# Optimization experiments

Hardware: AMD Instinct MI355X
Metric: run time of the kernel (lower is better)

The kernel has to match this reference:

```python
import jax, jax.numpy as jnp
import numpy as np

EPS = 1e-9


def _pairwise_sqdist(x1, x2):
    # x1: (B,n,3), x2: (B,m,3) -> (B,n,m) squared euclidean distances
    s1 = jnp.sum(x1 * x1, axis=-1)
    s2 = jnp.sum(x2 * x2, axis=-1)
    cross = jnp.einsum('bnd,bmd->bnm', x1, x2)
    return jnp.maximum(s1[:, :, None] + s2[:, None, :] - 2.0 * cross, 0.0)


def _approxmatch(x1, x2):
    # Faithful port of the approxmatch CUDA kernel (Fan et al. EMD approx).
    B, n, _ = x1.shape
    m = x2.shape[1]
    if n >= m:
        multiL, multiR = 1.0, float(n // m)   # integer division as in CUDA
    else:
        multiL, multiR = float(m // n), 1.0
    dist = _pairwise_sqdist(x1, x2)  # (B,n,m)
    # j = 7 .. -1 -> level = -4^j ; j = -2 -> level = 0  (10 sweeps total)
    levels = jnp.concatenate([
        -(4.0 ** jnp.arange(7, -2, -1, dtype=jnp.float32)),
        jnp.zeros((1,), jnp.float32)])
    match0 = jnp.zeros((B, n, m), jnp.float32)
    remainL0 = jnp.full((B, n), multiL, jnp.float32)
    remainR0 = jnp.full((B, m), multiR, jnp.float32)

    def body(carry, level):
        match, remainL, remainR = carry
        e = jnp.exp(level * dist)                              # (B,n,m)
        suml = EPS + jnp.einsum('bnm,bm->bn', e, remainR)
        ratioL = remainL / suml                                # (B,n)
        sumr = remainR * jnp.einsum('bnm,bn->bm', e, ratioL)   # (B,m)
        consumption = jnp.minimum(remainR / (sumr + EPS), 1.0)
        ratioR = consumption * remainR                         # (B,m)
        remainR = jnp.maximum(0.0, remainR - sumr)
        w = e * ratioL[:, :, None] * ratioR[:, None, :]        # flow k->l
        match = match + w
        remainL = jnp.maximum(0.0, remainL - jnp.sum(w, axis=-1))
        return (match, remainL, remainR), None

    (match, _, _), _ = jax.lax.scan(body, (match0, remainL0, remainR0), levels)
    return match, dist


def setup_inputs() -> dict:
    key = jax.random.key(0)
    k1, k2 = jax.random.split(key)
    B, N = 4, 4096
    xyz1 = jax.random.normal(k1, (B, 3, N), dtype=jnp.float32)
    xyz2 = jax.random.normal(k2, (B, 3, N), dtype=jnp.float32)
    return {"xyz1": xyz1, "xyz2": xyz2}


def reference(xyz1, xyz2):
    # transpose=True: BCN -> BNC
    x1 = jnp.transpose(xyz1, (0, 2, 1))
    x2 = jnp.transpose(xyz2, (0, 2, 1))
    match, dist = _approxmatch(x1, x2)
    d = jnp.sqrt(jnp.maximum(dist, 1e-20))
    cost = jnp.sum(match * d, axis=(1, 2))            # (B,)
    emd = cost / min(x1.shape[1], x2.shape[1])
    return jnp.mean(emd)                               # reduce_mean=True
```

## Files before the change

kernel.cpp:

```cpp
#include <hip/hip_runtime.h>


#define NPTS 4096
#define BATCH 4
#define EMD_EPS 1e-9f
#define TILE 1024
#define RPW 2
#define THREADS 256
#define RPB 8
#define NBLK (NPTS / RPB)

typedef float v2f __attribute__((ext_vector_type(2)));

__device__ __forceinline__ float fexp2(float x) {
#if __has_builtin(__builtin_amdgcn_exp2f)
    return __builtin_amdgcn_exp2f(x);
#else
    return exp2f(x);
#endif
}
__device__ __forceinline__ float fsqrt(float x) {
#if __has_builtin(__builtin_amdgcn_sqrtf)
    return __builtin_amdgcn_sqrtf(x);
#else
    return __sqrtf(x);
#endif
}

__device__ __forceinline__ float wave_reduce(float v) {
    v += __shfl_xor(v, 32);
    v += __shfl_xor(v, 16);
    v += __shfl_xor(v, 8);
    v += __shfl_xor(v, 4);
    v += __shfl_xor(v, 2);
    v += __shfl_xor(v, 1);
    return v;
}

__global__ __launch_bounds__(THREADS, 6) void k_ratioL0(
        const float* __restrict__ xyz1, const float* __restrict__ xyz2,
        float* __restrict__ ratioL, float* __restrict__ remainL,
        float* __restrict__ remainR, float ls2) {
    const int b = blockIdx.y;
    const int tid = threadIdx.x;
    const int wave = tid >> 6;
    const int lane = tid & 63;
    const int row0 = blockIdx.x * RPB + wave * RPW;

    const float* x1 = xyz1 + b * 3 * NPTS;
    const float* x2 = xyz2 + b * 3 * NPTS;
    const float2* x2x = (const float2*)(x2);
    const float2* x2y = (const float2*)(x2 + NPTS);
    const float2* x2z = (const float2*)(x2 + 2 * NPTS);

    float px[RPW], py[RPW], pz[RPW];
    v2f acc[RPW];
#pragma unroll
    for (int r = 0; r < RPW; ++r) {
        px[r] = x1[row0 + r];
        py[r] = x1[NPTS + row0 + r];
        pz[r] = x1[2 * NPTS + row0 + r];
        acc[r] = (v2f)(0.0f);
    }
    __shared__ float4 sA[TILE / 2];
    __shared__ float2 sZ[TILE / 2];

    for (int c0 = 0; c0 < NPTS; c0 += TILE) {
        __syncthreads();
        for (int i = tid; i < TILE / 2; i += THREADS) {
            int e = c0 / 2 + i;
            float2 xx = x2x[e], yy = x2y[e];
            sA[i] = make_float4(xx.x, xx.y, yy.x, yy.y);
            sZ[i] = x2z[e];
        }
        __syncthreads();
#pragma unroll 2
        for (int j = 0; j < TILE / 128; ++j) {
            float4 a = sA[lane + 64 * j];
            float2 z = sZ[lane + 64 * j];
            v2f ax = {a.x, a.y}, ay = {a.z, a.w}, az = {z.x, z.y};
#pragma unroll
            for (int r = 0; r < RPW; ++r) {
                v2f dx = px[r] - ax, dy = py[r] - ay, dz = pz[r] - az;
                v2f d = dx * dx + dy * dy + dz * dz;
                v2f sd = ls2 * d;
                v2f e2 = {fexp2(sd.x), fexp2(sd.y)};
                acc[r] += e2;
            }
        }
    }
#pragma unroll
    for (int r = 0; r < RPW; ++r) {
        float s = wave_reduce(acc[r].x + acc[r].y);
        if (lane == 0) {
            int idx = b * NPTS + row0 + r;
            ratioL[idx] = 1.0f / (EMD_EPS + s);
            remainL[idx] = 1.0f;
            remainR[idx] = 1.0f;
        }
    }
}

__global__ __launch_bounds__(THREADS, 6) void k_ratioR(
        const float* __restrict__ xyz1, const float* __restrict__ xyz2,
        const float* __restrict__ ratioL, float* __restrict__ ratioR,
        float* __restrict__ remainR, float ls2) {
    const int b = blockIdx.y;
    const int tid = threadIdx.x;
    const int wave = tid >> 6;
    const int lane = tid & 63;
    const int col0 = blockIdx.x * RPB + wave * RPW;

    const float* x1 = xyz1 + b * 3 * NPTS;
    const float* x2 = xyz2 + b * 3 * NPTS;
    const float2* x1x = (const float2*)(x1);
    const float2* x1y = (const float2*)(x1 + NPTS);
    const float2* x1z = (const float2*)(x1 + 2 * NPTS);
    const float2* wLv = (const float2*)(ratioL + b * NPTS);

    float px[RPW], py[RPW], pz[RPW];
    v2f acc[RPW];
#pragma unroll
    for (int r = 0; r < RPW; ++r) {
        px[r] = x2[col0 + r];
        py[r] = x2[NPTS + col0 + r];
        pz[r] = x2[2 * NPTS + col0 + r];
        acc[r] = (v2f)(0.0f);
    }
    __shared__ float4 sA[TILE / 2];
    __shared__ float4 sB[TILE / 2];

    for (int c0 = 0; c0 < NPTS; c0 += TILE) {
        __syncthreads();
        for (int i = tid; i < TILE / 2; i += THREADS) {
            int e = c0 / 2 + i;
            float2 xx = x1x[e], yy = x1y[e], zz = x1z[e], ww = wLv[e];
            sA[i] = make_float4(xx.x, xx.y, yy.x, yy.y);
            sB[i] = make_float4(zz.x, zz.y, ww.x, ww.y);
        }
        __syncthreads();
#pragma unroll 2
        for (int j = 0; j < TILE / 128; ++j) {
            float4 a = sA[lane + 64 * j];
            float4 bq = sB[lane + 64 * j];
            v2f ax = {a.x, a.y}, ay = {a.z, a.w};
            v2f az = {bq.x, bq.y}, aw = {bq.z, bq.w};
#pragma unroll
            for (int r = 0; r < RPW; ++r) {
                v2f dx = px[r] - ax, dy = py[r] - ay, dz = pz[r] - az;
                v2f d = dx * dx + dy * dy + dz * dz;
                v2f sd = ls2 * d;
                v2f e2 = {fexp2(sd.x), fexp2(sd.y)};
                acc[r] += e2 * aw;
            }
        }
    }
#pragma unroll
    for (int r = 0; r < RPW; ++r) {
        float s = wave_reduce(acc[r].x + acc[r].y);
        if (lane == 0) {
            int idx = b * NPTS + col0 + r;
            float rv = remainR[idx];
            float sumr = rv * s;
            float cons = fminf(rv / (sumr + EMD_EPS), 1.0f);
            ratioR[idx] = cons * rv;
            remainR[idx] = fmaxf(0.0f, rv - sumr);
        }
    }
}

template <bool SQ>
__global__ __launch_bounds__(THREADS, 6) void k_cost_fused(
        const float* __restrict__ xyz1, const float* __restrict__ xyz2,
        float* __restrict__ ratioL, const float* __restrict__ ratioR,
        float* __restrict__ remainL, const float* __restrict__ remainR,
        float* __restrict__ cost_part, float ls2, float ls2n, int initCost) {
    const int b = blockIdx.y;
    const int tid = threadIdx.x;
    const int wave = tid >> 6;
    const int lane = tid & 63;
    const int row0 = blockIdx.x * RPB + wave * RPW;

    const float* x1 = xyz1 + b * 3 * NPTS;
    const float* x2 = xyz2 + b * 3 * NPTS;
    const float2* x2x = (const float2*)(x2);
    const float2* x2y = (const float2*)(x2 + NPTS);
    const float2* x2z = (const float2*)(x2 + 2 * NPTS);
    const float2* wRv = (const float2*)(ratioR + b * NPTS);
    const float2* w2v = (const float2*)(remainR + b * NPTS);

    float px[RPW], py[RPW], pz[RPW];
    v2f acc_a[RPW], acc_c[RPW], acc_s[RPW];
#pragma unroll
    for (int r = 0; r < RPW; ++r) {
        px[r] = x1[row0 + r];
        py[r] = x1[NPTS + row0 + r];
        pz[r] = x1[2 * NPTS + row0 + r];
        acc_a[r] = (v2f)(0.0f);
        acc_c[r] = (v2f)(0.0f);
        acc_s[r] = (v2f)(0.0f);
    }
    __shared__ float4 sA[TILE / 2];
    __shared__ float4 sB[TILE / 2];
    __shared__ float2 sC[TILE / 2];
    __shared__ float s_cost[THREADS / 64];

    for (int c0 = 0; c0 < NPTS; c0 += TILE) {
        __syncthreads();
        for (int i = tid; i < TILE / 2; i += THREADS) {
            int e = c0 / 2 + i;
            float2 xx = x2x[e], yy = x2y[e], zz = x2z[e], wr = wRv[e];
            sA[i] = make_float4(xx.x, xx.y, yy.x, yy.y);
            sB[i] = make_float4(zz.x, zz.y, wr.x, wr.y);
            sC[i] = w2v[e];
        }
        __syncthreads();
#pragma unroll 2
        for (int j = 0; j < TILE / 128; ++j) {
            float4 a = sA[lane + 64 * j];
            float4 bq = sB[lane + 64 * j];
            float2 c = sC[lane + 64 * j];
            v2f ax = {a.x, a.y}, ay = {a.z, a.w};
            v2f az = {bq.x, bq.y}, wr = {bq.z, bq.w};
            v2f cw = {c.x, c.y};
#pragma unroll
            for (int r = 0; r < RPW; ++r) {
                v2f dx = px[r] - ax, dy = py[r] - ay, dz = pz[r] - az;
                v2f d = dx * dx + dy * dy + dz * dz;
                v2f er;
                if (SQ) {
                    v2f sd = ls2n * d;
                    v2f e2 = {fexp2(sd.x), fexp2(sd.y)};
                    acc_s[r] += e2 * cw;
                    v2f e4 = e2 * e2;
                    er = (e4 * e4) * wr;
                } else {
                    v2f sd = ls2 * d;
                    v2f e1 = {fexp2(sd.x), fexp2(sd.y)};
                    er = e1 * wr;
                    acc_s[r] += cw;
                }
                acc_a[r] += er;
                v2f sq = {fsqrt(d.x), fsqrt(d.y)};
                acc_c[r] += er * sq;
            }
        }
    }
    float wcost = 0.0f;
#pragma unroll
    for (int r = 0; r < RPW; ++r) {
        float sa = wave_reduce(acc_a[r].x + acc_a[r].y);
        float sc = wave_reduce(acc_c[r].x + acc_c[r].y);
        float ss = wave_reduce(acc_s[r].x + acc_s[r].y);
        if (lane == 0) {
            int idx = b * NPTS + row0 + r;
            float rl = ratioL[idx];
            float rem = fmaxf(0.0f, remainL[idx] - rl * sa);
            remainL[idx] = rem;
            ratioL[idx] = rem / (EMD_EPS + ss);
            wcost = fmaf(rl, sc, wcost);
        }
    }
    if (lane == 0) s_cost[wave] = wcost;
    __syncthreads();
    if (tid == 0) {
        float t = s_cost[0] + s_cost[1] + s_cost[2] + s_cost[3];
        int ci = b * NBLK + blockIdx.x;
        cost_part[ci] = (initCost ? t : cost_part[ci] + t);
    }
}

__global__ void k_sum_ratioL(const float* __restrict__ ratioL, float* __restrict__ S_L) {
    const int b = blockIdx.x;
    const int tid = threadIdx.x;
    float s = 0.0f;
    for (int i = tid; i < NPTS; i += 256) s += ratioL[b * NPTS + i];
    s = wave_reduce(s);
    __shared__ float sw[4];
    if ((tid & 63) == 0) sw[tid >> 6] = s;
    __syncthreads();
    if (tid == 0) S_L[b] = sw[0] + sw[1] + sw[2] + sw[3];
}

__global__ __launch_bounds__(THREADS, 6) void k_cost_l0(
        const float* __restrict__ xyz1, const float* __restrict__ xyz2,
        const float* __restrict__ ratioL, const float* __restrict__ remainR,
        const float* __restrict__ S_L, float* __restrict__ cost_part) {
    const int b = blockIdx.y;
    const int tid = threadIdx.x;
    const int wave = tid >> 6;
    const int lane = tid & 63;
    const int row0 = blockIdx.x * RPB + wave * RPW;
    const float sL = S_L[b];

    const float* x1 = xyz1 + b * 3 * NPTS;
    const float* x2 = xyz2 + b * 3 * NPTS;
    const float2* x2x = (const float2*)(x2);
    const float2* x2y = (const float2*)(x2 + NPTS);
    const float2* x2z = (const float2*)(x2 + 2 * NPTS);
    const float2* wRv = (const float2*)(remainR + b * NPTS);

    float px[RPW], py[RPW], pz[RPW];
    v2f acc_c[RPW];
#pragma unroll
    for (int r = 0; r < RPW; ++r) {
        px[r] = x1[row0 + r];
        py[r] = x1[NPTS + row0 + r];
        pz[r] = x1[2 * NPTS + row0 + r];
        acc_c[r] = (v2f)(0.0f);
    }
    __shared__ float4 sA[TILE / 2];
    __shared__ float4 sB[TILE / 2];
    __shared__ float s_cost[THREADS / 64];

    for (int c0 = 0; c0 < NPTS; c0 += TILE) {
        __syncthreads();
        for (int i = tid; i < TILE / 2; i += THREADS) {
            int e = c0 / 2 + i;
            float2 xx = x2x[e], yy = x2y[e], zz = x2z[e], rv = wRv[e];
            float wr0 = fminf(rv.x / (rv.x * sL + EMD_EPS), 1.0f) * rv.x;
            float wr1 = fminf(rv.y / (rv.y * sL + EMD_EPS), 1.0f) * rv.y;
            sA[i] = make_float4(xx.x, xx.y, yy.x, yy.y);
            sB[i] = make_float4(zz.x, zz.y, wr0, wr1);
        }
        __syncthreads();
#pragma unroll 2
        for (int j = 0; j < TILE / 128; ++j) {
            float4 a = sA[lane + 64 * j];
            float4 bq = sB[lane + 64 * j];
            v2f ax = {a.x, a.y}, ay = {a.z, a.w};
            v2f az = {bq.x, bq.y}, wr = {bq.z, bq.w};
#pragma unroll
            for (int r = 0; r < RPW; ++r) {
                v2f dx = px[r] - ax, dy = py[r] - ay, dz = pz[r] - az;
                v2f d = dx * dx + dy * dy + dz * dz;
                v2f sq = {fsqrt(d.x), fsqrt(d.y)};
                acc_c[r] += wr * sq;
            }
        }
    }
    float wcost = 0.0f;
#pragma unroll
    for (int r = 0; r < RPW; ++r) {
        float sc = wave_reduce(acc_c[r].x + acc_c[r].y);
        if (lane == 0)
            wcost = fmaf(ratioL[b * NPTS + row0 + r], sc, wcost);
    }
    if (lane == 0) s_cost[wave] = wcost;
    __syncthreads();
    if (tid == 0) {
        float t = s_cost[0] + s_cost[1] + s_cost[2] + s_cost[3];
        cost_part[b * NBLK + blockIdx.x] += t;
    }
}

__global__ void k_final(const float* __restrict__ cost_part, float* __restrict__ out) {
    const int tid = threadIdx.x;
    float s = 0.0f;
    for (int i = tid; i < BATCH * NBLK; i += 256) s += cost_part[i];
    s = wave_reduce(s);
    __shared__ float sw[4];
    if ((tid & 63) == 0) sw[tid >> 6] = s;
    __syncthreads();
    if (tid == 0) out[0] = (sw[0] + sw[1] + sw[2] + sw[3]) / ((float)NPTS * (float)BATCH);
}

extern "C" void kernel_launch(void* const* d_in, const int* in_sizes, int n_in,
                              void* d_out, int out_size, void* d_ws, size_t ws_size,
                              hipStream_t stream) {
    const float* xyz1 = (const float*)d_in[0];
    const float* xyz2 = (const float*)d_in[1];
    float* out = (float*)d_out;

    const int BN = BATCH * NPTS;
    float* ws = (float*)d_ws;
    float* remainL  = ws;
    float* remainR  = ws + 1 * BN;
    float* ratioL   = ws + 2 * BN;
    float* ratioR   = ws + 3 * BN;
    float* cost_part = ws + 4 * BN;
    float* S_L      = cost_part + BATCH * NBLK;

    static const float levels[10] = {
        -16384.0f, -4096.0f, -1024.0f, -256.0f, -64.0f,
        -16.0f, -4.0f, -1.0f, -0.25f, 0.0f};
    float ls2[10];
    for (int t = 0; t < 10; ++t)
        ls2[t] = (float)(levels[t] * 1.4426950408889634);

    dim3 grid(NBLK, BATCH);

    k_ratioL0<<<grid, THREADS, 0, stream>>>(xyz1, xyz2, ratioL, remainL, remainR, ls2[0]);
    for (int t = 0; t < 8; ++t) {
        k_ratioR<<<grid, THREADS, 0, stream>>>(xyz1, xyz2, ratioL, ratioR, remainR, ls2[t]);
        k_cost_fused<true><<<grid, THREADS, 0, stream>>>(xyz1, xyz2, ratioL, ratioR,
                                                         remainL, remainR, cost_part,
                                                         ls2[t], ls2[t + 1], t == 0 ? 1 : 0);
    }
    k_ratioR<<<grid, THREADS, 0, stream>>>(xyz1, xyz2, ratioL, ratioR, remainR, ls2[8]);
    k_cost_fused<false><<<grid, THREADS, 0, stream>>>(xyz1, xyz2, ratioL, ratioR,
                                                      remainL, remainR, cost_part,
                                                      ls2[8], 0.0f, 0);
    k_sum_ratioL<<<BATCH, 256, 0, stream>>>(ratioL, S_L);
    k_cost_l0<<<grid, THREADS, 0, stream>>>(xyz1, xyz2, ratioL, remainR, S_L, cost_part);
    k_final<<<1, 256, 0, stream>>>(cost_part, out);
}
```

Baseline: 565.4 us.

## Cull negligible exp terms wave-wide and double rows per wave

Adds wave-uniform culling of exp2 evaluations in the first few high-magnitude level sweeps: when every lane's scaled distance is below a threshold, the exp, and optionally the cost and sqrt terms, are skipped because they would underflow to zero or be negligible. Separately, rows per wave go from 2 to 4 (rows per block 8 to 16), which improves reuse of the shared-memory tiles, and launch bounds are relaxed to 4 blocks per CU. The partial cull threshold drops terms that are small but not exactly zero, which slightly changes numerics. The extra per-step wave votes add branch overhead when little can be culled.

After: 527.5 us. 1.07x faster.

```diff
diff --git a/kernel.cpp b/kernel.cpp
--- a/kernel.cpp
+++ b/kernel.cpp
@@ -5,10 +5,13 @@
 #define BATCH 4
 #define EMD_EPS 1e-9f
 #define TILE 1024
-#define RPW 2
+#define RPW 4
 #define THREADS 256
-#define RPB 8
+#define RPB 16
 #define NBLK (NPTS / RPB)
+
+#define CULL_FULL -160.0f
+#define CULL_PART -40.0f
 
 typedef float v2f __attribute__((ext_vector_type(2)));
 
@@ -37,7 +40,7 @@
     return v;
 }
 
-__global__ __launch_bounds__(THREADS, 6) void k_ratioL0(
+__global__ __launch_bounds__(THREADS, 4) void k_ratioL0(
         const float* __restrict__ xyz1, const float* __restrict__ xyz2,
         float* __restrict__ ratioL, float* __restrict__ remainL,
         float* __restrict__ remainR, float ls2) {
@@ -84,8 +87,10 @@
                 v2f dx = px[r] - ax, dy = py[r] - ay, dz = pz[r] - az;
                 v2f d = dx * dx + dy * dy + dz * dz;
                 v2f sd = ls2 * d;
-                v2f e2 = {fexp2(sd.x), fexp2(sd.y)};
-                acc[r] += e2;
+                if (!__all(fmaxf(sd.x, sd.y) < CULL_FULL)) {
+                    v2f e2 = {fexp2(sd.x), fexp2(sd.y)};
+                    acc[r] += e2;
+                }
             }
         }
     }
@@ -101,7 +106,8 @@
     }
 }
 
-__global__ __launch_bounds__(THREADS, 6) void k_ratioR(
+template <bool CULL>
+__global__ __launch_bounds__(THREADS, 4) void k_ratioR(
         const float* __restrict__ xyz1, const float* __restrict__ xyz2,
         const float* __restrict__ ratioL, float* __restrict__ ratioR,
         float* __restrict__ remainR, float ls2) {
@@ -150,8 +156,12 @@
                 v2f dx = px[r] - ax, dy = py[r] - ay, dz = pz[r] - az;
                 v2f d = dx * dx + dy * dy + dz * dz;
                 v2f sd = ls2 * d;
-                v2f e2 = {fexp2(sd.x), fexp2(sd.y)};
-                acc[r] += e2 * aw;
+                bool live = true;
+                if (CULL) live = !__all(fmaxf(sd.x, sd.y) < CULL_FULL);
+                if (live) {
+                    v2f e2 = {fexp2(sd.x), fexp2(sd.y)};
+                    acc[r] += e2 * aw;
+                }
             }
         }
     }
@@ -169,8 +179,8 @@
     }
 }
 
-template <bool SQ>
-__global__ __launch_bounds__(THREADS, 6) void k_cost_fused(
+template <bool SQ, bool CULL>
+__global__ __launch_bounds__(THREADS, 4) void k_cost_fused(
         const float* __restrict__ xyz1, const float* __restrict__ xyz2,
         float* __restrict__ ratioL, const float* __restrict__ ratioR,
         float* __restrict__ remainL, const float* __restrict__ remainR,
@@ -227,22 +237,34 @@
             for (int r = 0; r < RPW; ++r) {
                 v2f dx = px[r] - ax, dy = py[r] - ay, dz = pz[r] - az;
                 v2f d = dx * dx + dy * dy + dz * dz;
-                v2f er;
                 if (SQ) {
                     v2f sd = ls2n * d;
-                    v2f e2 = {fexp2(sd.x), fexp2(sd.y)};
-                    acc_s[r] += e2 * cw;
-                    v2f e4 = e2 * e2;
-                    er = (e4 * e4) * wr;
+                    bool fullskip = false, partskip = false;
+                    if (CULL) {
+                        float mx = fmaxf(sd.x, sd.y);
+                        fullskip = __all(mx < CULL_FULL);
+                        partskip = __all(mx < CULL_PART);
+                    }
+                    if (!fullskip) {
+                        v2f e2 = {fexp2(sd.x), fexp2(sd.y)};
+                        acc_s[r] += e2 * cw;
+                        if (!partskip) {
+                            v2f e4 = e2 * e2;
+                            v2f er = (e4 * e4) * wr;
+                            acc_a[r] += er;
+                            v2f sq = {fsqrt(d.x), fsqrt(d.y)};
+                            acc_c[r] += er * sq;
+                        }
+                    }
                 } else {
                     v2f sd = ls2 * d;
                     v2f e1 = {fexp2(sd.x), fexp2(sd.y)};
-                    er = e1 * wr;
+                    v2f er = e1 * wr;
                     acc_s[r] += cw;
+                    acc_a[r] += er;
+                    v2f sq = {fsqrt(d.x), fsqrt(d.y)};
+                    acc_c[r] += er * sq;
                 }
-                acc_a[r] += er;
-                v2f sq = {fsqrt(d.x), fsqrt(d.y)};
-                acc_c[r] += er * sq;
             }
         }
     }
@@ -282,7 +304,7 @@
     if (tid == 0) S_L[b] = sw[0] + sw[1] + sw[2] + sw[3];
 }
 
-__global__ __launch_bounds__(THREADS, 6) void k_cost_l0(
+__global__ __launch_bounds__(THREADS, 4) void k_cost_l0(
         const float* __restrict__ xyz1, const float* __restrict__ xyz2,
         const float* __restrict__ ratioL, const float* __restrict__ remainR,
         const float* __restrict__ S_L, float* __restrict__ cost_part) {
@@ -392,15 +414,24 @@
 
     k_ratioL0<<<grid, THREADS, 0, stream>>>(xyz1, xyz2, ratioL, remainL, remainR, ls2[0]);
     for (int t = 0; t < 8; ++t) {
-        k_ratioR<<<grid, THREADS, 0, stream>>>(xyz1, xyz2, ratioL, ratioR, remainR, ls2[t]);
-        k_cost_fused<true><<<grid, THREADS, 0, stream>>>(xyz1, xyz2, ratioL, ratioR,
-                                                         remainL, remainR, cost_part,
-                                                         ls2[t], ls2[t + 1], t == 0 ? 1 : 0);
-    }
-    k_ratioR<<<grid, THREADS, 0, stream>>>(xyz1, xyz2, ratioL, ratioR, remainR, ls2[8]);
-    k_cost_fused<false><<<grid, THREADS, 0, stream>>>(xyz1, xyz2, ratioL, ratioR,
-                                                      remainL, remainR, cost_part,
-                                                      ls2[8], 0.0f, 0);
+        if (t < 3) {
+            k_ratioR<true><<<grid, THREADS, 0, stream>>>(xyz1, xyz2, ratioL, ratioR,
+                                                         remainR, ls2[t]);
+            k_cost_fused<true, true><<<grid, THREADS, 0, stream>>>(
+                xyz1, xyz2, ratioL, ratioR, remainL, remainR, cost_part,
+                ls2[t], ls2[t + 1], t == 0 ? 1 : 0);
+        } else {
+            k_ratioR<false><<<grid, THREADS, 0, stream>>>(xyz1, xyz2, ratioL, ratioR,
+                                                          remainR, ls2[t]);
+            k_cost_fused<true, false><<<grid, THREADS, 0, stream>>>(
+                xyz1, xyz2, ratioL, ratioR, remainL, remainR, cost_part,
+                ls2[t], ls2[t + 1], 0);
+        }
+    }
+    k_ratioR<false><<<grid, THREADS, 0, stream>>>(xyz1, xyz2, ratioL, ratioR,
+                                                  remainR, ls2[8]);
+    k_cost_fused<false, false><<<grid, THREADS, 0, stream>>>(
+        xyz1, xyz2, ratioL, ratioR, remainL, remainR, cost_part, ls2[8], 0.0f, 0);
     k_sum_ratioL<<<BATCH, 256, 0, stream>>>(ratioL, S_L);
     k_cost_l0<<<grid, THREADS, 0, stream>>>(xyz1, xyz2, ratioL, remainR, S_L, cost_part);
     k_final<<<1, 256, 0, stream>>>(cost_part, out);
```
